# Performance work log

Hardware: AMD Instinct MI355X
Metric: run time of the kernel (lower is better)

Reference implementation:

```python
import jax, jax.numpy as jnp
import numpy as np

# Dropout layers are treated as identity (eval mode); note the original Adaptive
# module references self.dropout without defining it, so train mode would error anyway.

def setup_inputs() -> dict:
    key = jax.random.key(0)
    ks = jax.random.split(key, 13)
    B, T, H, E2, VOC, K = 128, 64, 512, 1024, 10000, 49
    s = lambda *sh: 1.0 / np.sqrt(sh[-1])
    return {
        "x":       jax.random.normal(ks[0], (B, T, E2), jnp.float32),
        "hiddens": jax.random.normal(ks[1], (B, T, H), jnp.float32),
        "cells":   jax.random.normal(ks[2], (B, T, H), jnp.float32),
        "V":       jax.random.normal(ks[3], (B, K, H), jnp.float32),
        # attention params
        "Wv": jax.random.normal(ks[4], (K, H), jnp.float32) * s(K, H),
        "Wg": jax.random.normal(ks[5], (K, H), jnp.float32) * s(K, H),
        "Ws": jax.random.normal(ks[6], (K, H), jnp.float32) * s(K, H),
        "wh": jax.random.normal(ks[7], (K,), jnp.float32) * s(K,),
        # sentinel params
        "Wx":  jax.random.normal(ks[8], (H, E2), jnp.float32) * s(H, E2),
        "Wsh": jax.random.normal(ks[9], (H, H), jnp.float32) * s(H, H),
        # output mlp
        "Wm": jax.random.normal(ks[10], (VOC, H), jnp.float32) * s(VOC, H),
        "bm": jnp.zeros((VOC,), jnp.float32),
    }


def reference(x, hiddens, cells, V, Wv, Wg, Ws, wh, Wx, Wsh, Wm, bm):
    B, T, H = hiddens.shape
    # h_{t-1}: zero init state prepended, last hidden dropped
    h0 = jnp.zeros((B, 1, H), hiddens.dtype)
    hiddens_t_1 = jnp.concatenate([h0, hiddens[:, :-1, :]], axis=1) if T > 1 else h0

    # Sentinel gate: sent_t = sigmoid(x Wx^T + h_{t-1} Wh^T) * tanh(cells)
    gate = jnp.einsum('bte,he->bth', x, Wx) + jnp.einsum('btj,hj->bth', hiddens_t_1, Wsh)
    sent = jax.nn.sigmoid(gate) * jnp.tanh(cells)            # [B,T,H]

    # Additive attention over K=49 spatial features
    cv = jnp.einsum('bkh,nh->bkn', V, Wv)                    # [B,K,49]
    cg = jnp.einsum('bth,nh->btn', hiddens, Wg)              # [B,T,49]
    content = jnp.tanh(cv[:, None, :, :] + cg[:, :, None, :])  # [B,T,K,49]
    z = jnp.einsum('btkn,n->btk', content, wh)               # [B,T,K]
    alpha = jax.nn.softmax(z, axis=-1)                       # [B,T,K]
    c = jnp.einsum('btk,bkh->bth', alpha, V)                 # [B,T,H]

    # Sentinel-extended softmax -> beta
    cs = jnp.einsum('bth,nh->btn', sent, Ws) + cg            # [B,T,49]
    z_ext = jnp.einsum('btn,n->bt', jnp.tanh(cs), wh)[..., None]  # [B,T,1]
    extend = jnp.concatenate([z, z_ext], axis=-1)            # [B,T,K+1]
    alpha_hat = jax.nn.softmax(extend, axis=-1)
    beta = alpha_hat[:, :, -1:]                              # [B,T,1]

    c_hat = beta * sent + (1.0 - beta) * c                   # [B,T,H]
    output = jnp.einsum('bth,vh->btv', c_hat + hiddens, Wm) + bm  # [B,T,vocab]
    return output, alpha, beta
```

## Files before the change

kernel.cpp:

```cpp
#include <hip/hip_runtime.h>
#include <hip/hip_bf16.h>
#include <math.h>

typedef __bf16 bf16;
typedef __bf16 bf16x4 __attribute__((ext_vector_type(4)));
typedef __bf16 bf16x8 __attribute__((ext_vector_type(8)));
typedef float f32x4 __attribute__((ext_vector_type(4)));

#define BB  128
#define TT  64
#define BTT 8192
#define HH  512
#define EE  1024
#define KA  49
#define NV  10000

__device__ __forceinline__ float ftanh(float x) {
    float cx = fminf(fmaxf(x, -15.f), 15.f);
    float e = __expf(2.f * cx);
    return (e - 1.f) * __builtin_amdgcn_rcpf(e + 1.f);
}
__device__ __forceinline__ float fsigmoid(float x) {
    return __builtin_amdgcn_rcpf(1.f + __expf(-x));
}

__device__ __forceinline__ void cvt4(const float* __restrict__ s, bf16* __restrict__ d) {
    f32x4 v = *(const f32x4*)s;
    bf16x4 o = { (bf16)v[0], (bf16)v[1], (bf16)v[2], (bf16)v[3] };
    *(bf16x4*)d = o;
}
__device__ __forceinline__ void cvt4nt(const float* __restrict__ s, bf16* __restrict__ d) {
    f32x4 v = __builtin_nontemporal_load((const f32x4*)s);
    bf16x4 o = { (bf16)v[0], (bf16)v[1], (bf16)v[2], (bf16)v[3] };
    *(bf16x4*)d = o;
}

__global__ __launch_bounds__(256)
void prep_kernel(const float* __restrict__ x, const float* __restrict__ hid,
                 const float* __restrict__ V, const float* __restrict__ Wv,
                 const float* __restrict__ Wg, const float* __restrict__ Ws,
                 const float* __restrict__ Wx, const float* __restrict__ Wsh,
                 bf16* __restrict__ xb, bf16* __restrict__ hb,
                 bf16* __restrict__ Vb, bf16* __restrict__ Wvb, bf16* __restrict__ Wgb,
                 bf16* __restrict__ Wsb, bf16* __restrict__ Wxb, bf16* __restrict__ Wshb,
                 bf16* __restrict__ zbuf)
{
    if (blockIdx.x == 0 && threadIdx.x < 128) {
        bf16x8 z = {};
        *(bf16x8*)(zbuf + threadIdx.x * 8) = z;
    }

    const long NX = (long)BTT * EE;
    const long NH = (long)BTT * HH;
    const long NVV = (long)BB * KA * HH;
    const long NWX = (long)HH * EE;
    const long NWSH = (long)HH * HH;
    const long NW = (long)KA * HH;
    const long total4 = (NX + NH + NVV + NWX + NWSH + 3 * NW) >> 2;

    long t0 = (long)blockIdx.x * 256 + threadIdx.x;
    long st = (long)gridDim.x * 256;
    for (long i4 = t0; i4 < total4; i4 += st) {
        long i = i4 << 2;
        if (i < NX) { cvt4nt(x + i, xb + i); continue; }
        i -= NX;
        if (i < NH) { cvt4(hid + i, hb + i); continue; }
        i -= NH;
        if (i < NVV) { cvt4nt(V + i, Vb + i); continue; }
        i -= NVV;
        if (i < NWX) { cvt4nt(Wx + i, Wxb + i); continue; }
        i -= NWX;
        if (i < NWSH) { cvt4nt(Wsh + i, Wshb + i); continue; }
        i -= NWSH;
        if (i < NW) { cvt4nt(Wv + i, Wvb + i); continue; }
        i -= NW;
        if (i < NW) { cvt4nt(Wg + i, Wgb + i); continue; }
        i -= NW;
        cvt4nt(Ws + i, Wsb + i);
    }
}

template<int EPI, bool SHIFT>
__device__ __forceinline__ void gemm128_core(
    bf16* smem,
    const bf16* __restrict__ A1, const bf16* __restrict__ B1, int K1,
    const bf16* __restrict__ A2, const bf16* __restrict__ B2, int K2,
    int N, const float* __restrict__ eaux, void* __restrict__ outv, int ldo,
    int bm0, int bn0, const bf16* __restrict__ zbuf)
{
    const int tid = threadIdx.x;
    const int lane = tid & 63;
    const int wid = tid >> 6;
    const int wm = (wid >> 1) * 64;
    const int wn = (wid & 1) * 64;
    const int rA = lane & 15;
    const int ks = lane >> 4;
    const int swzB = (ks ^ ((rA >> 1) & 3)) * 16;

    const int c0 = tid, c1 = tid + 256;
    const int row0 = c0 >> 2, row1 = c1 >> 2;
    const int gc0 = ((c0 & 3) ^ ((row0 >> 1) & 3)) * 8;
    const int gc1 = ((c1 & 3) ^ ((row1 >> 1) & 3)) * 8;
    const int br0 = (bn0 + row0 < N) ? bn0 + row0 : N - 1;
    const int br1 = (bn0 + row1 < N) ? bn0 + row1 : N - 1;

    const int NT1 = K1 >> 5;
    const int NT2 = K2 >> 5;
    const int NT = NT1 + NT2;

    const bf16* A1r0 = A1 + (size_t)(bm0 + row0) * K1 + gc0;
    const bf16* A1r1 = A1 + (size_t)(bm0 + row1) * K1 + gc1;
    const bf16* B1r0 = B1 + (size_t)br0 * K1 + gc0;
    const bf16* B1r1 = B1 + (size_t)br1 * K1 + gc1;
    const bf16 *A2r0 = nullptr, *A2r1 = nullptr, *B2r0 = nullptr, *B2r1 = nullptr;
    if (K2 > 0) {
        if (SHIFT) {
            A2r0 = (((bm0 + row0) & 63) == 0) ? zbuf + gc0
                                              : A2 + (size_t)(bm0 + row0 - 1) * K2 + gc0;
            A2r1 = (((bm0 + row1) & 63) == 0) ? zbuf + gc1
                                              : A2 + (size_t)(bm0 + row1 - 1) * K2 + gc1;
        } else {
            A2r0 = A2 + (size_t)(bm0 + row0) * K2 + gc0;
            A2r1 = A2 + (size_t)(bm0 + row1) * K2 + gc1;
        }
        B2r0 = B2 + (size_t)br0 * K2 + gc0;
        B2r1 = B2 + (size_t)br1 * K2 + gc1;
    }

    auto stage = [&](int t) {
        const bf16 *a0, *a1, *b0, *b1; int k0;
        if (t < NT1) { k0 = t << 5;          a0 = A1r0; a1 = A1r1; b0 = B1r0; b1 = B1r1; }
        else         { k0 = (t - NT1) << 5;  a0 = A2r0; a1 = A2r1; b0 = B2r0; b1 = B2r1; }
        char* base = (char*)smem + (t & 3) * 16384;
        __builtin_amdgcn_global_load_lds(
            (const __attribute__((address_space(1))) unsigned int*)(a0 + k0),
            (__attribute__((address_space(3))) unsigned int*)(base + c0 * 16), 16, 0, 0);
        __builtin_amdgcn_global_load_lds(
            (const __attribute__((address_space(1))) unsigned int*)(a1 + k0),
            (__attribute__((address_space(3))) unsigned int*)(base + c1 * 16), 16, 0, 0);
        __builtin_amdgcn_global_load_lds(
            (const __attribute__((address_space(1))) unsigned int*)(b0 + k0),
            (__attribute__((address_space(3))) unsigned int*)(base + 8192 + c0 * 16), 16, 0, 0);
        __builtin_amdgcn_global_load_lds(
            (const __attribute__((address_space(1))) unsigned int*)(b1 + k0),
            (__attribute__((address_space(3))) unsigned int*)(base + 8192 + c1 * 16), 16, 0, 0);
    };

    f32x4 acc[4][4] = {};

    stage(0); stage(1); stage(2);
    asm volatile("s_waitcnt vmcnt(8)" ::: "memory");
    __builtin_amdgcn_s_barrier();

    for (int t = 0; t < NT; ++t) {
        const char* sA = (const char*)smem + (t & 3) * 16384;
        const char* sB = sA + 8192;

        bf16x8 af[4], bfr[4];
        #pragma unroll
        for (int mi = 0; mi < 4; ++mi)
            af[mi] = *(const bf16x8*)(sA + (wm + mi * 16 + rA) * 64 + swzB);
        #pragma unroll
        for (int ni = 0; ni < 4; ++ni)
            bfr[ni] = *(const bf16x8*)(sB + (wn + ni * 16 + rA) * 64 + swzB);

        if (t + 3 < NT) {
            stage(t + 3);
            asm volatile("s_waitcnt vmcnt(8)" ::: "memory");
        } else if (t + 2 < NT) {
            asm volatile("s_waitcnt vmcnt(4)" ::: "memory");
        } else {
            asm volatile("s_waitcnt vmcnt(0)" ::: "memory");
        }
        __builtin_amdgcn_s_barrier();

        __builtin_amdgcn_s_setprio(1);
        #pragma unroll
        for (int mi = 0; mi < 4; ++mi) {
            #pragma unroll
            for (int ni = 0; ni < 4; ++ni)
                acc[mi][ni] = __builtin_amdgcn_mfma_f32_16x16x32_bf16(af[mi], bfr[ni], acc[mi][ni], 0, 0, 0);
        }
        __builtin_amdgcn_s_setprio(0);
        __builtin_amdgcn_s_barrier();
    }

    #pragma unroll
    for (int mi = 0; mi < 4; ++mi) {
        #pragma unroll
        for (int ni = 0; ni < 4; ++ni) {
            const int col = bn0 + wn + ni * 16 + rA;
            if (col < N) {
                #pragma unroll
                for (int r = 0; r < 4; ++r) {
                    const int rowg = bm0 + wm + mi * 16 + ks * 4 + r;
                    float v = acc[mi][ni][r];
                    if (EPI == 0) {
                        ((bf16*)outv)[(size_t)rowg * ldo + col] =
                            (bf16)(fsigmoid(v) * ftanh(eaux[(size_t)rowg * ldo + col]));
                    } else {
                        ((float*)outv)[(size_t)rowg * ldo + col] = v;
                    }
                }
            }
        }
    }
}

__global__ __launch_bounds__(256, 2)
void gate_mid128(const bf16* __restrict__ xb, const bf16* __restrict__ Wxb,
                 const bf16* __restrict__ Wshb,
                 const float* __restrict__ cel, bf16* __restrict__ sentb,
                 const bf16* __restrict__ Vb, const bf16* __restrict__ Wvb,
                 const bf16* __restrict__ hb, const bf16* __restrict__ Wgb,
                 float* __restrict__ cv, float* __restrict__ cg,
                 const float* __restrict__ Wm, bf16* __restrict__ Wmb,
                 const bf16* __restrict__ zbuf)
{
    __shared__ bf16 smem[4 * 8192];
    const int bid = blockIdx.x;
    if (bid >= 369) {
        const long n4 = ((long)NV * HH) >> 2;
        for (long i4 = (long)(bid - 369) * 256 + threadIdx.x; i4 < n4; i4 += 143L * 256)
            cvt4nt(Wm + (i4 << 2), Wmb + (i4 << 2));
        return;
    }
    if (bid < 256) {
        const int bm0 = (bid >> 2) * 128;
        const int bn0 = (bid & 3) * 128;
        gemm128_core<0, true>(smem, xb, Wxb, EE, hb, Wshb, HH, HH, cel, (void*)sentb, HH,
                              bm0, bn0, zbuf);
    } else if (bid < 305) {
        gemm128_core<2, false>(smem, Vb, Wvb, HH, nullptr, nullptr, 0, KA, nullptr,
                               (void*)cv, KA, (bid - 256) * 128, 0, nullptr);
    } else {
        gemm128_core<2, false>(smem, hb, Wgb, HH, nullptr, nullptr, 0, KA, nullptr,
                               (void*)cg, KA, (bid - 305) * 128, 0, nullptr);
    }
}

__global__ __launch_bounds__(256, 2)
void cs128(const bf16* __restrict__ sentb, const bf16* __restrict__ Wsb,
           const bf16* __restrict__ hb, const bf16* __restrict__ Wgb,
           float* __restrict__ cs)
{
    __shared__ bf16 smem[4 * 8192];
    gemm128_core<2, false>(smem, sentb, Wsb, HH, hb, Wgb, HH, KA, nullptr, (void*)cs, KA,
                           blockIdx.x * 128, 0, nullptr);
}

__global__ __launch_bounds__(512, 4)
void gemm256x128_bias(const bf16* __restrict__ A, const bf16* __restrict__ B,
                      const float* __restrict__ bias, float* __restrict__ out)
{
    const int K = HH;
    const int N = NV;
    const int NT = K / 32;
    const int ntn = 79;

    __shared__ bf16 smem[3 * 12288];

    const int bid = blockIdx.x;
    const int wg = (bid & 7) * 316 + (bid >> 3);
    const int bm0 = (wg / ntn) * 256;
    const int bn0 = (wg % ntn) * 128;

    const int tid = threadIdx.x;
    const int lane = tid & 63;
    const int wid = tid >> 6;
    const int wr = (wid >> 1) * 64;
    const int wc = (wid & 1) * 64;
    const int rA = lane & 15;
    const int ks = lane >> 4;
    const int swz = (ks ^ ((rA >> 1) & 3)) * 16;

    const int arow0 = tid >> 2;
    const int arow1 = arow0 + 128;
    const int gcA0 = ((tid & 3) ^ ((arow0 >> 1) & 3)) * 8;
    const int gcA1 = ((tid & 3) ^ ((arow1 >> 1) & 3)) * 8;
    const int brow = tid >> 2;
    const int gcB  = ((tid & 3) ^ ((brow >> 1) & 3)) * 8;
    const int browc = (bn0 + brow < N) ? bn0 + brow : N - 1;

    const bf16* Ap0 = A + (size_t)(bm0 + arow0) * K + gcA0;
    const bf16* Ap1 = A + (size_t)(bm0 + arow1) * K + gcA1;
    const bf16* Bp  = B + (size_t)browc * K + gcB;

    auto stage = [&](int t, int slot) {
        char* base = (char*)smem + slot * 24576;
        const int k0 = t << 5;
        __builtin_amdgcn_global_load_lds(
            (const __attribute__((address_space(1))) unsigned int*)(Ap0 + k0),
            (__attribute__((address_space(3))) unsigned int*)(base + tid * 16), 16, 0, 0);
        __builtin_amdgcn_global_load_lds(
            (const __attribute__((address_space(1))) unsigned int*)(Ap1 + k0),
            (__attribute__((address_space(3))) unsigned int*)(base + (tid + 512) * 16), 16, 0, 0);
        __builtin_amdgcn_global_load_lds(
            (const __attribute__((address_space(1))) unsigned int*)(Bp + k0),
            (__attribute__((address_space(3))) unsigned int*)(base + 16384 + tid * 16), 16, 0, 0);
    };

    f32x4 acc[4][4] = {};

    stage(0, 0); stage(1, 1);
    asm volatile("s_waitcnt vmcnt(3)" ::: "memory");
    __builtin_amdgcn_s_barrier();

    int slR = 0, slS = 2;
    for (int t = 0; t < NT; ++t) {
        const char* sA = (const char*)smem + slR * 24576;
        const char* sB = sA + 16384;

        bf16x8 af[4], bfr[4];
        #pragma unroll
        for (int mi = 0; mi < 4; ++mi)
            af[mi] = *(const bf16x8*)(sA + (wr + mi * 16 + rA) * 64 + swz);
        #pragma unroll
        for (int ni = 0; ni < 4; ++ni)
            bfr[ni] = *(const bf16x8*)(sB + (wc + ni * 16 + rA) * 64 + swz);

        if (t + 2 < NT) {
            stage(t + 2, slS);
            asm volatile("s_waitcnt vmcnt(3)" ::: "memory");
        } else {
            asm volatile("s_waitcnt vmcnt(0)" ::: "memory");
        }
        __builtin_amdgcn_s_barrier();

        __builtin_amdgcn_s_setprio(1);
        #pragma unroll
        for (int mi = 0; mi < 4; ++mi) {
            #pragma unroll
            for (int ni = 0; ni < 4; ++ni)
                acc[mi][ni] = __builtin_amdgcn_mfma_f32_16x16x32_bf16(af[mi], bfr[ni], acc[mi][ni], 0, 0, 0);
        }
        __builtin_amdgcn_s_setprio(0);
        __builtin_amdgcn_s_barrier();

        slR = (slR == 2) ? 0 : slR + 1;
        slS = (slS == 2) ? 0 : slS + 1;
    }

    float bv[4];
    #pragma unroll
    for (int ni = 0; ni < 4; ++ni) {
        const int col = bn0 + wc + ni * 16 + rA;
        bv[ni] = (col < N) ? bias[col] : 0.f;
    }
    float* lt = (float*)smem + wid * 2048;
    #pragma unroll
    for (int half = 0; half < 2; ++half) {
        #pragma unroll
        for (int mi2 = 0; mi2 < 2; ++mi2) {
            const int mi = half * 2 + mi2;
            #pragma unroll
            for (int ni = 0; ni < 4; ++ni) {
                #pragma unroll
                for (int r = 0; r < 4; ++r) {
                    const int row = mi2 * 16 + ks * 4 + r;
                    const int col = ni * 16 + rA;
                    const int s = ((((row >> 2) & 3) ^ (row & 3)) << 4);
                    lt[row * 64 + (col ^ s)] = acc[mi][ni][r] + bv[ni];
                }
            }
        }
        #pragma unroll
        for (int i = 0; i < 8; ++i) {
            const int row = i * 4 + ks;
            const int c0 = rA * 4;
            const int s = ((((row >> 2) & 3) ^ (row & 3)) << 4);
            f32x4 v = *(const f32x4*)&lt[row * 64 + (c0 ^ s)];
            const int rowg = bm0 + wr + half * 32 + row;
            const int colg = bn0 + wc + c0;
            if (colg < N)
                __builtin_nontemporal_store(v, (f32x4*)&out[(size_t)rowg * N + colg]);
        }
    }
}

__global__ __launch_bounds__(256)
void softz_kernel(const float* __restrict__ cv, const float* __restrict__ cg,
                  const float* __restrict__ cs, const float* __restrict__ wh,
                  float* __restrict__ alpha, float* __restrict__ beta)
{
    __shared__ float cvL[KA * KA];
    __shared__ float whL[64];
    __shared__ float cgL[4 * KA];

    const int tid = threadIdx.x;
    const int w = tid >> 6, lane = tid & 63;
    const int bt0 = blockIdx.x * 4;
    const int b = bt0 >> 6;
    const int bt = bt0 + w;

    const float* cvb = cv + (size_t)b * KA * KA;
    for (int i = tid; i < KA * KA; i += 256) cvL[i] = cvb[i];
    if (tid < KA) whL[tid] = wh[tid];
    if (lane < KA) cgL[w * KA + lane] = cg[(size_t)bt * KA + lane];
    float csv = (lane < KA) ? cs[(size_t)bt * KA + lane] : 0.f;
    __syncthreads();

    float z = -INFINITY;
    if (lane < KA) {
        const float* cvk = cvL + lane * KA;
        const float* cgr = cgL + w * KA;
        float acc = 0.f;
        #pragma unroll 7
        for (int n = 0; n < KA; ++n)
            acc += ftanh(cvk[n] + cgr[n]) * whL[n];
        z = acc;
    }
    float u = (lane < KA) ? ftanh(csv) * whL[lane] : 0.f;

    float m1 = z;
    #pragma unroll
    for (int o = 32; o; o >>= 1) m1 = fmaxf(m1, __shfl_xor(m1, o, 64));
    float e = (lane < KA) ? __expf(z - m1) : 0.f;
    float s1 = e, ze = u;
    #pragma unroll
    for (int o = 32; o; o >>= 1) { s1 += __shfl_xor(s1, o, 64); ze += __shfl_xor(ze, o, 64); }

    if (lane < KA) alpha[(size_t)bt * KA + lane] = e / s1;
    if (lane == 0) {
        float M2 = fmaxf(m1, ze);
        float denom = s1 * __expf(m1 - M2) + __expf(ze - M2);
        beta[bt] = __expf(ze - M2) / denom;
    }
}

__global__ __launch_bounds__(256)
void cch_kernel(const float* __restrict__ alpha, const float* __restrict__ beta,
                const bf16* __restrict__ Vb, const bf16* __restrict__ sentb,
                const float* __restrict__ hid, bf16* __restrict__ chb)
{
    __shared__ float aL[TT * KA];
    __shared__ float bL[TT];

    const int b = blockIdx.x >> 3;
    const int hc = blockIdx.x & 7;
    const int tid = threadIdx.x;
    const int w = tid >> 6, lane = tid & 63;
    const int h = hc * 64 + lane;

    const float* ab = alpha + (size_t)b * TT * KA;
    for (int i = tid; i < TT * KA; i += 256) aL[i] = ab[i];
    if (tid < TT) bL[tid] = beta[b * TT + tid];

    float vreg[KA];
    #pragma unroll
    for (int k = 0; k < KA; ++k) vreg[k] = (float)Vb[((size_t)b * KA + k) * HH + h];
    __syncthreads();

    #pragma unroll 1
    for (int tt = 0; tt < 16; ++tt) {
        const int t = w * 16 + tt;
        const int bt = b * TT + t;
        const float* ar = aL + t * KA;
        float c = 0.f;
        #pragma unroll
        for (int k = 0; k < KA; ++k) c += ar[k] * vreg[k];
        const float be = bL[t];
        const size_t idx = (size_t)bt * HH + h;
        float ch = be * (float)sentb[idx] + (1.f - be) * c
                 + __builtin_nontemporal_load(hid + idx);
        chb[idx] = (bf16)ch;
    }
}

extern "C" void kernel_launch(void* const* d_in, const int* in_sizes, int n_in,
                              void* d_out, int out_size, void* d_ws, size_t ws_size,
                              hipStream_t stream)
{
    const float* x   = (const float*)d_in[0];
    const float* hid = (const float*)d_in[1];
    const float* cel = (const float*)d_in[2];
    const float* V   = (const float*)d_in[3];
    const float* Wv  = (const float*)d_in[4];
    const float* Wg  = (const float*)d_in[5];
    const float* Ws  = (const float*)d_in[6];
    const float* wh  = (const float*)d_in[7];
    const float* Wx  = (const float*)d_in[8];
    const float* Wsh = (const float*)d_in[9];
    const float* Wm  = (const float*)d_in[10];
    const float* bm  = (const float*)d_in[11];

    float* out_o   = (float*)d_out;
    float* alpha_o = out_o + (size_t)BTT * NV;
    float* beta_o  = alpha_o + (size_t)BTT * KA;

    char* p = (char*)d_ws;
    bf16* sentb = (bf16*)p; p += (size_t)BTT * HH * 2;
    bf16* chb   = (bf16*)p; p += (size_t)BTT * HH * 2;
    bf16* xb    = (bf16*)p; p += (size_t)BTT * EE * 2;
    bf16* hb    = (bf16*)p; p += (size_t)BTT * HH * 2;
    bf16* Vb    = (bf16*)p; p += (size_t)BB * KA * HH * 2;
    bf16* Wxb   = (bf16*)p; p += (size_t)HH * EE * 2;
    bf16* Wshb  = (bf16*)p; p += (size_t)HH * HH * 2;
    bf16* Wmb   = (bf16*)p; p += (size_t)NV * HH * 2;
    bf16* Wvb   = (bf16*)p; p += (size_t)KA * HH * 2;
    bf16* Wgb   = (bf16*)p; p += (size_t)KA * HH * 2;
    bf16* Wsb   = (bf16*)p; p += (size_t)KA * HH * 2;
    bf16* zbuf  = (bf16*)p; p += 1024 * 2;
    float* cv   = (float*)p; p += (size_t)BB * KA * KA * 4;
    float* cg   = (float*)p; p += (size_t)BTT * KA * 4;
    float* cs   = (float*)p; p += (size_t)BTT * KA * 4;

    prep_kernel<<<2048, 256, 0, stream>>>(x, hid, V, Wv, Wg, Ws, Wx, Wsh,
                                          xb, hb, Vb, Wvb, Wgb, Wsb, Wxb, Wshb, zbuf);

    gate_mid128<<<512, 256, 0, stream>>>(xb, Wxb, Wshb, cel, sentb,
                                         Vb, Wvb, hb, Wgb, cv, cg, Wm, Wmb, zbuf);

    cs128<<<64, 256, 0, stream>>>(sentb, Wsb, hb, Wgb, cs);

    softz_kernel<<<BTT / 4, 256, 0, stream>>>(cv, cg, cs, wh, alpha_o, beta_o);
    cch_kernel<<<BB * 8, 256, 0, stream>>>(alpha_o, beta_o, Vb, sentb, hid, chb);

    gemm256x128_bias<<<32 * 79, 512, 0, stream>>>(chb, Wmb, bm, out_o);
}
```

Measured before the change: 226.8 us.

## Fuse cs GEMM, attention softmax and context blend into one kernel

Replaces three kernels (cs128 GEMM, softz_kernel, cch_kernel) with a single fused_mid kernel in which each block handles 32 timesteps of one batch. The block computes the sentinel projection with MFMA from LDS-resident sent tiles, then the attention softmax and beta, and finally the context blend using V and sent already staged in LDS. This removes two launches and the global round trips of cs and of alpha/beta, and avoids re-reading sentb. In exchange it uses about 126KB of LDS and only 256 blocks at one block per CU, which limits latency hiding and parallelism.

Measured after the change: 240.2 us. 5.9% more time.

```diff
diff --git a/kernel.cpp b/kernel.cpp
--- a/kernel.cpp
+++ b/kernel.cpp
@@ -239,14 +239,152 @@
     }
 }
 
-__global__ __launch_bounds__(256, 2)
-void cs128(const bf16* __restrict__ sentb, const bf16* __restrict__ Wsb,
-           const bf16* __restrict__ hb, const bf16* __restrict__ Wgb,
-           float* __restrict__ cs)
+__global__ __launch_bounds__(256, 1)
+void fused_mid(const float* __restrict__ cv, const float* __restrict__ cg,
+               const float* __restrict__ wh, const bf16* __restrict__ sentb,
+               const bf16* __restrict__ Wsb, const bf16* __restrict__ Vb,
+               const float* __restrict__ hid, float* __restrict__ alpha,
+               float* __restrict__ beta, bf16* __restrict__ chb)
 {
-    __shared__ bf16 smem[4 * 8192];
-    gemm128_core<2, false>(smem, sentb, Wsb, HH, hb, Wgb, HH, KA, nullptr, (void*)cs, KA,
-                           blockIdx.x * 128, 0, nullptr);
+    __shared__ char Lm[128968];
+    bf16* sentL = (bf16*)Lm;
+    char* WsL   = Lm + 32768;
+    bf16* VL    = (bf16*)(Lm + 32768);
+    float* csL  = (float*)(Lm + 98304);
+    float* cvL  = (float*)(Lm + 106496);
+    float* cgL  = (float*)(Lm + 116100);
+    float* alphaL = (float*)(Lm + 122372);
+    float* whL  = (float*)(Lm + 128644);
+    float* bL   = (float*)(Lm + 128840);
+
+    const int bid = blockIdx.x;
+    const int b = bid >> 1;
+    const int r0 = b * 64 + (bid & 1) * 32;
+    const int tid = threadIdx.x;
+    const int lane = tid & 63;
+    const int wid = tid >> 6;
+
+    #pragma unroll
+    for (int i = 0; i < 8; ++i) {
+        const int cgk = tid + i * 256;
+        const int kt = cgk >> 7, c = cgk & 127;
+        const int row = c >> 2, slot = c & 3;
+        const int gcol = kt * 32 + ((slot ^ ((row >> 1) & 3)) * 8);
+        __builtin_amdgcn_global_load_lds(
+            (const __attribute__((address_space(1))) unsigned int*)(sentb + (size_t)(r0 + row) * HH + gcol),
+            (__attribute__((address_space(3))) unsigned int*)((char*)sentL + kt * 2048 + c * 16), 16, 0, 0);
+    }
+    #pragma unroll
+    for (int i = 0; i < 16; ++i) {
+        const int cgk = tid + i * 256;
+        const int kt = cgk >> 8, c = cgk & 255;
+        const int row = c >> 2, slot = c & 3;
+        const int rowc = (row < KA) ? row : KA - 1;
+        const int gcol = kt * 32 + ((slot ^ ((row >> 1) & 3)) * 8);
+        __builtin_amdgcn_global_load_lds(
+            (const __attribute__((address_space(1))) unsigned int*)(Wsb + (size_t)rowc * HH + gcol),
+            (__attribute__((address_space(3))) unsigned int*)(WsL + kt * 4096 + c * 16), 16, 0, 0);
+    }
+    asm volatile("s_waitcnt vmcnt(0)" ::: "memory");
+    __builtin_amdgcn_s_barrier();
+
+    const int wm = wid >> 1, wn = wid & 1;
+    const int rA = lane & 15, ks = lane >> 4;
+    const int swz = (ks ^ ((rA >> 1) & 3)) * 16;
+    f32x4 acc2[2] = {};
+    #pragma unroll
+    for (int kt = 0; kt < 16; ++kt) {
+        bf16x8 af = *(const bf16x8*)((char*)sentL + kt * 2048 + (wm * 16 + rA) * 64 + swz);
+        #pragma unroll
+        for (int ni = 0; ni < 2; ++ni) {
+            bf16x8 bf_ = *(const bf16x8*)(WsL + kt * 4096 + (wn * 32 + ni * 16 + rA) * 64 + swz);
+            acc2[ni] = __builtin_amdgcn_mfma_f32_16x16x32_bf16(af, bf_, acc2[ni], 0, 0, 0);
+        }
+    }
+    #pragma unroll
+    for (int ni = 0; ni < 2; ++ni) {
+        #pragma unroll
+        for (int r = 0; r < 4; ++r) {
+            const int row = wm * 16 + ks * 4 + r;
+            const int col = wn * 32 + ni * 16 + rA;
+            csL[row * 64 + col] = acc2[ni][r];
+        }
+    }
+    __syncthreads();
+
+    for (int i = 0; i < 13; ++i) {
+        const int c = tid + i * 256;
+        if (c < (KA * HH * 2) / 16) {
+            __builtin_amdgcn_global_load_lds(
+                (const __attribute__((address_space(1))) unsigned int*)(Vb + (size_t)b * KA * HH + c * 8),
+                (__attribute__((address_space(3))) unsigned int*)((char*)VL + c * 16), 16, 0, 0);
+        }
+    }
+    for (int i = tid; i < KA * KA; i += 256) cvL[i] = cv[(size_t)b * KA * KA + i];
+    for (int i = tid; i < 32 * KA; i += 256) cgL[i] = cg[(size_t)r0 * KA + i];
+    if (tid < KA) whL[tid] = wh[tid];
+    __syncthreads();
+
+    for (int j = 0; j < 8; ++j) {
+        const int t = wid * 8 + j;
+        float z = -INFINITY;
+        if (lane < KA) {
+            const float* cvk = cvL + lane * KA;
+            const float* cgr = cgL + t * KA;
+            float a = 0.f;
+            #pragma unroll 7
+            for (int n = 0; n < KA; ++n)
+                a += ftanh(cvk[n] + cgr[n]) * whL[n];
+            z = a;
+        }
+        const float csv = (lane < KA) ? csL[t * 64 + lane] + cgL[t * KA + lane] : 0.f;
+        float u = (lane < KA) ? ftanh(csv) * whL[lane] : 0.f;
+
+        float m1 = z;
+        #pragma unroll
+        for (int o = 32; o; o >>= 1) m1 = fmaxf(m1, __shfl_xor(m1, o, 64));
+        float e = (lane < KA) ? __expf(z - m1) : 0.f;
+        float s1 = e, ze = u;
+        #pragma unroll
+        for (int o = 32; o; o >>= 1) { s1 += __shfl_xor(s1, o, 64); ze += __shfl_xor(ze, o, 64); }
+
+        if (lane < KA) {
+            const float av = e / s1;
+            alpha[(size_t)(r0 + t) * KA + lane] = av;
+            alphaL[t * KA + lane] = av;
+        }
+        if (lane == 0) {
+            const float M2 = fmaxf(m1, ze);
+            const float denom = s1 * __expf(m1 - M2) + __expf(ze - M2);
+            const float bv = __expf(ze - M2) / denom;
+            beta[r0 + t] = bv;
+            bL[t] = bv;
+        }
+    }
+    __syncthreads();
+
+    #pragma unroll
+    for (int hc = 0; hc < 2; ++hc) {
+        const int h = hc * 256 + tid;
+        float vreg[KA];
+        #pragma unroll
+        for (int k = 0; k < KA; ++k) vreg[k] = (float)VL[k * HH + h];
+        const int kt = h >> 5, gslot = (h >> 3) & 3, off = h & 7;
+        #pragma unroll 4
+        for (int t = 0; t < 32; ++t) {
+            const float* ar = alphaL + t * KA;
+            float c = 0.f;
+            #pragma unroll
+            for (int k = 0; k < KA; ++k) c += ar[k] * vreg[k];
+            const float be = bL[t];
+            const size_t idx = (size_t)(r0 + t) * HH + h;
+            const bf16 sv = *(const bf16*)((char*)sentL + kt * 2048 + t * 64 +
+                                           ((gslot ^ ((t >> 1) & 3)) * 16) + off * 2);
+            const float ch = be * (float)sv + (1.f - be) * c
+                           + __builtin_nontemporal_load(hid + idx);
+            chb[idx] = (bf16)ch;
+        }
+    }
 }
 
 __global__ __launch_bounds__(512, 4)
@@ -375,95 +513,6 @@
             if (colg < N)
                 __builtin_nontemporal_store(v, (f32x4*)&out[(size_t)rowg * N + colg]);
         }
-    }
-}
-
-__global__ __launch_bounds__(256)
-void softz_kernel(const float* __restrict__ cv, const float* __restrict__ cg,
-                  const float* __restrict__ cs, const float* __restrict__ wh,
-                  float* __restrict__ alpha, float* __restrict__ beta)
-{
-    __shared__ float cvL[KA * KA];
-    __shared__ float whL[64];
-    __shared__ float cgL[4 * KA];
-
-    const int tid = threadIdx.x;
-    const int w = tid >> 6, lane = tid & 63;
-    const int bt0 = blockIdx.x * 4;
-    const int b = bt0 >> 6;
-    const int bt = bt0 + w;
-
-    const float* cvb = cv + (size_t)b * KA * KA;
-    for (int i = tid; i < KA * KA; i += 256) cvL[i] = cvb[i];
-    if (tid < KA) whL[tid] = wh[tid];
-    if (lane < KA) cgL[w * KA + lane] = cg[(size_t)bt * KA + lane];
-    float csv = (lane < KA) ? cs[(size_t)bt * KA + lane] : 0.f;
-    __syncthreads();
-
-    float z = -INFINITY;
-    if (lane < KA) {
-        const float* cvk = cvL + lane * KA;
-        const float* cgr = cgL + w * KA;
-        float acc = 0.f;
-        #pragma unroll 7
-        for (int n = 0; n < KA; ++n)
-            acc += ftanh(cvk[n] + cgr[n]) * whL[n];
-        z = acc;
-    }
-    float u = (lane < KA) ? ftanh(csv) * whL[lane] : 0.f;
-
-    float m1 = z;
-    #pragma unroll
-    for (int o = 32; o; o >>= 1) m1 = fmaxf(m1, __shfl_xor(m1, o, 64));
-    float e = (lane < KA) ? __expf(z - m1) : 0.f;
-    float s1 = e, ze = u;
-    #pragma unroll
-    for (int o = 32; o; o >>= 1) { s1 += __shfl_xor(s1, o, 64); ze += __shfl_xor(ze, o, 64); }
-
-    if (lane < KA) alpha[(size_t)bt * KA + lane] = e / s1;
-    if (lane == 0) {
-        float M2 = fmaxf(m1, ze);
-        float denom = s1 * __expf(m1 - M2) + __expf(ze - M2);
-        beta[bt] = __expf(ze - M2) / denom;
-    }
-}
-
-__global__ __launch_bounds__(256)
-void cch_kernel(const float* __restrict__ alpha, const float* __restrict__ beta,
-                const bf16* __restrict__ Vb, const bf16* __restrict__ sentb,
-                const float* __restrict__ hid, bf16* __restrict__ chb)
-{
-    __shared__ float aL[TT * KA];
-    __shared__ float bL[TT];
-
-    const int b = blockIdx.x >> 3;
-    const int hc = blockIdx.x & 7;
-    const int tid = threadIdx.x;
-    const int w = tid >> 6, lane = tid & 63;
-    const int h = hc * 64 + lane;
-
-    const float* ab = alpha + (size_t)b * TT * KA;
-    for (int i = tid; i < TT * KA; i += 256) aL[i] = ab[i];
-    if (tid < TT) bL[tid] = beta[b * TT + tid];
-
-    float vreg[KA];
-    #pragma unroll
-    for (int k = 0; k < KA; ++k) vreg[k] = (float)Vb[((size_t)b * KA + k) * HH + h];
-    __syncthreads();
-
-    #pragma unroll 1
-    for (int tt = 0; tt < 16; ++tt) {
-        const int t = w * 16 + tt;
-        const int bt = b * TT + t;
-        const float* ar = aL + t * KA;
-        float c = 0.f;
-        #pragma unroll
-        for (int k = 0; k < KA; ++k) c += ar[k] * vreg[k];
-        const float be = bL[t];
-        const size_t idx = (size_t)bt * HH + h;
-        float ch = be * (float)sentb[idx] + (1.f - be) * c
-                 + __builtin_nontemporal_load(hid + idx);
-        chb[idx] = (bf16)ch;
     }
 }
 
@@ -503,7 +552,6 @@
     bf16* zbuf  = (bf16*)p; p += 1024 * 2;
     float* cv   = (float*)p; p += (size_t)BB * KA * KA * 4;
     float* cg   = (float*)p; p += (size_t)BTT * KA * 4;
-    float* cs   = (float*)p; p += (size_t)BTT * KA * 4;
 
     prep_kernel<<<2048, 256, 0, stream>>>(x, hid, V, Wv, Wg, Ws, Wx, Wsh,
                                           xb, hb, Vb, Wvb, Wgb, Wsb, Wxb, Wshb, zbuf);
@@ -511,10 +559,8 @@
     gate_mid128<<<512, 256, 0, stream>>>(xb, Wxb, Wshb, cel, sentb,
                                          Vb, Wvb, hb, Wgb, cv, cg, Wm, Wmb, zbuf);
 
-    cs128<<<64, 256, 0, stream>>>(sentb, Wsb, hb, Wgb, cs);
-
-    softz_kernel<<<BTT / 4, 256, 0, stream>>>(cv, cg, cs, wh, alpha_o, beta_o);
-    cch_kernel<<<BB * 8, 256, 0, stream>>>(alpha_o, beta_o, Vb, sentb, hid, chb);
+    fused_mid<<<256, 256, 0, stream>>>(cv, cg, wh, sentb, Wsb, Vb, hid,
+                                       alpha_o, beta_o, chb);
 
     gemm256x128_bias<<<32 * 79, 512, 0, stream>>>(chb, Wmb, bm, out_o);
 }
```
